# Performance work log

Measured on AMD Instinct MI355X. Metric: run time of the kernel, lower is better.

The kernel has to match this reference:

```python
import jax, jax.numpy as jnp
import numpy as np

N_HEAD = 12
N_EMBD = 768
HEAD_DIM = N_EMBD // N_HEAD
B, S = 4, 2048


def setup_inputs() -> dict:
    key = jax.random.key(0)
    k1, k2, k3, k4, k5 = jax.random.split(key, 5)
    x = jax.random.normal(k1, (B, S, N_EMBD), dtype=jnp.float32)
    # causal additive mask: 1.0 where attention is disallowed (strictly upper triangle)
    mask = (1.0 - jnp.tril(jnp.ones((S, S), dtype=jnp.float32)))[None, None, :, :]
    scale = 0.02
    W_attn = jax.random.normal(k2, (N_EMBD, 3 * N_EMBD), dtype=jnp.float32) * scale
    b_attn = jnp.zeros((3 * N_EMBD,), dtype=jnp.float32)
    W_proj = jax.random.normal(k3, (N_EMBD, N_EMBD), dtype=jnp.float32) * scale
    b_proj = jnp.zeros((N_EMBD,), dtype=jnp.float32)
    return {"x": x, "mask": mask, "W_attn": W_attn, "b_attn": b_attn,
            "W_proj": W_proj, "b_proj": b_proj}


def reference(x, mask, W_attn, b_attn, W_proj, b_proj):
    Bn, Sn, _ = x.shape
    qkv = x @ W_attn + b_attn                      # [B,S,3E]
    q, k, v = jnp.split(qkv, 3, axis=-1)           # each [B,S,E]

    def heads(t):
        return t.reshape(Bn, Sn, N_HEAD, HEAD_DIM).transpose(0, 2, 1, 3)  # [B,H,S,D]

    q, k, v = heads(q), heads(k), heads(v)
    attn = jnp.einsum('bhqd,bhkd->bhqk', q, k) / jnp.sqrt(jnp.float32(HEAD_DIM))
    attn = attn + mask * (-1e9)
    attn = jax.nn.softmax(attn, axis=-1)
    # dropout in inference mode = identity
    out = jnp.einsum('bhqk,bhkd->bhqd', attn, v)   # [B,H,S,D]
    out = out.transpose(0, 2, 1, 3).reshape(Bn, Sn, N_EMBD)
    return out @ W_proj + b_proj
```

## Files before the change

kernel.cpp:

```cpp
#include <hip/hip_runtime.h>
#include <stdint.h>

#define NHEAD 12
#define HDIM  64
#define EMB   768
#define N3    2304
#define SEQ   2048
#define BATCH 4
#define MROWS 8192

#define QSCALE 0.18033688011112042f

typedef __bf16 bf16_t;
typedef __bf16 bf16x8 __attribute__((ext_vector_type(8)));
typedef __bf16 bf16x4 __attribute__((ext_vector_type(4)));
typedef short  s16x4  __attribute__((ext_vector_type(4)));
typedef float  f32x4  __attribute__((ext_vector_type(4)));

__device__ __forceinline__ void gld_lds16(void* lds, const void* g) {
    __builtin_amdgcn_global_load_lds((const __attribute__((address_space(1))) void*)g,
                                     (__attribute__((address_space(3))) void*)lds,
                                     16, 0, 0);
}

__device__ __forceinline__ float fast_exp2(float x) {
    return __builtin_amdgcn_exp2f(x);
}

__device__ __forceinline__ f32x4 mfma16_bf16(bf16x4 a, bf16x4 b, f32x4 c) {
#if __has_builtin(__builtin_amdgcn_mfma_f32_16x16x16_bf16)
    return __builtin_amdgcn_mfma_f32_16x16x16_bf16(a, b, c, 0, 0, 0);
#else
    union U { bf16x4 h; s16x4 s; };
    U ua, ub; ua.h = a; ub.h = b;
    return __builtin_amdgcn_mfma_f32_16x16x16bf16_1k(ua.s, ub.s, c, 0, 0, 0);
#endif
}

__global__ __launch_bounds__(256) void cvt_x_k(const float* __restrict__ x,
                                               bf16_t* __restrict__ xb, int n8) {
    int idx    = blockIdx.x * blockDim.x + threadIdx.x;
    int stride = gridDim.x * blockDim.x;
    for (int i = idx; i < n8; i += stride) {
        float4 a = ((const float4*)x)[i * 2];
        float4 b = ((const float4*)x)[i * 2 + 1];
        bf16x8 v;
        v[0] = (bf16_t)a.x; v[1] = (bf16_t)a.y; v[2] = (bf16_t)a.z; v[3] = (bf16_t)a.w;
        v[4] = (bf16_t)b.x; v[5] = (bf16_t)b.y; v[6] = (bf16_t)b.z; v[7] = (bf16_t)b.w;
        ((bf16x8*)xb)[i] = v;
    }
}

__global__ __launch_bounds__(256) void transpose_cvt_k(
    const float* __restrict__ W, bf16_t* __restrict__ WT, int K, int N) {
    __shared__ float tile[32][33];
    const int n0 = blockIdx.x * 32, k0 = blockIdx.y * 32;
    const int tx = threadIdx.x & 31, ty = threadIdx.x >> 5;
#pragma unroll
    for (int i = 0; i < 32; i += 8)
        tile[ty + i][tx] = W[(size_t)(k0 + ty + i) * N + (n0 + tx)];
    __syncthreads();
#pragma unroll
    for (int i = 0; i < 32; i += 8)
        WT[(size_t)(n0 + ty + i) * K + (k0 + tx)] = (bf16_t)tile[tx][ty + i];
}

template<int MODE>
__global__ __launch_bounds__(256) void gemm_kernel(
    const bf16_t* __restrict__ Av,
    const bf16_t* __restrict__ BT,
    const float* __restrict__ bias,
    float* __restrict__ out,
    bf16_t* __restrict__ qbuf,
    bf16_t* __restrict__ kbuf,
    bf16_t* __restrict__ vbuf,
    int Ncols)
{
    const int K = 768;
    __shared__ alignas(16) bf16_t As[2][128 * 32];
    __shared__ alignas(16) bf16_t Bs[2][128 * 32];

    const int tid    = threadIdx.x;
    const int wave   = tid >> 6;
    const int lane   = tid & 63;
    const int lane15 = lane & 15;
    const int quad   = lane >> 4;

    const int bid   = blockIdx.x;
    const int chunk = (int)(gridDim.x >> 3);
    const int swz   = (bid & 7) * chunk + (bid >> 3);
    const int NB    = Ncols >> 7;
    const int mBase = (swz / NB) * 128;
    const int nBase = (swz % NB) * 128;

    const int wm = (wave >> 1) * 64;
    const int wn = (wave & 1) * 64;

    f32x4 acc[4][4];
#pragma unroll
    for (int i = 0; i < 4; i++)
#pragma unroll
        for (int j = 0; j < 4; j++) acc[i][j] = (f32x4){0.f, 0.f, 0.f, 0.f};

    const bf16_t* aSrc = Av + (size_t)mBase * K;
    const bf16_t* bSrc = BT + (size_t)nBase * K;

    const int srow = lane >> 2;
    const int sch  = lane & 3;

    auto issueA = [&](int k0, int buf) {
#pragma unroll
        for (int p = 0; p < 2; p++) {
            int r0  = p * 64 + wave * 16;
            int row = r0 + srow;
            int lch = sch ^ (row & 3);
            gld_lds16(&As[buf][r0 * 32], aSrc + (size_t)row * K + k0 + lch * 8);
        }
    };
    auto issueB = [&](int k0, int buf) {
#pragma unroll
        for (int p = 0; p < 2; p++) {
            int r0  = p * 64 + wave * 16;
            int row = r0 + srow;
            int lch = sch ^ (row & 3);
            gld_lds16(&Bs[buf][r0 * 32], bSrc + (size_t)row * K + k0 + lch * 8);
        }
    };

    issueA(0, 0);
    issueB(0, 0);

    for (int k0 = 0, it = 0; k0 < K; k0 += 32, it++) {
        const int buf = it & 1;
        __syncthreads();
        if (k0 + 32 < K) {
            issueB(k0 + 32, buf ^ 1);
            issueA(k0 + 32, buf ^ 1);
        }

        bf16x8 aF[4], bF[4];
#pragma unroll
        for (int t = 0; t < 4; t++) {
            int ra = wm + t * 16 + lane15;
            int rb = wn + t * 16 + lane15;
            aF[t] = *(const bf16x8*)&As[buf][ra * 32 + (quad ^ (ra & 3)) * 8];
            bF[t] = *(const bf16x8*)&Bs[buf][rb * 32 + (quad ^ (rb & 3)) * 8];
        }
#pragma unroll
        for (int i = 0; i < 4; i++)
#pragma unroll
            for (int j = 0; j < 4; j++)
                acc[i][j] = __builtin_amdgcn_mfma_f32_16x16x32_bf16(aF[i], bF[j], acc[i][j], 0, 0, 0);
    }

    const int region = (MODE == 1) ? (nBase / EMB) : 0;
#pragma unroll
    for (int i = 0; i < 4; i++) {
#pragma unroll
        for (int j = 0; j < 4; j++) {
            int gn = nBase + wn + j * 16 + lane15;
            float bv = bias[gn];
            if (MODE == 0) {
#pragma unroll
                for (int r = 0; r < 4; r++) {
                    int gm = mBase + wm + i * 16 + quad * 4 + r;
                    out[(size_t)gm * Ncols + gn] = acc[i][j][r] + bv;
                }
            } else if (region == 2) {
                int within = gn - 2 * EMB;
                int h = within >> 6, d = within & 63;
                int gm0 = mBase + wm + i * 16 + quad * 4;
                int b = gm0 >> 11, s = gm0 & 2047;
                int bh = b * NHEAD + h;
                bf16x4 v4;
#pragma unroll
                for (int r = 0; r < 4; r++) v4[r] = (bf16_t)(acc[i][j][r] + bv);
                *(bf16x4*)&vbuf[((size_t)bh * HDIM + d) * SEQ + s] = v4;
            } else {
                bf16_t* dst = (region == 0) ? qbuf : kbuf;
                const float scale = (region == 0) ? QSCALE : 1.0f;
                int within = gn - region * EMB;
                int h = within >> 6, d = within & 63;
#pragma unroll
                for (int r = 0; r < 4; r++) {
                    int gm = mBase + wm + i * 16 + quad * 4 + r;
                    int b = gm >> 11, s = gm & 2047;
                    int bh = b * NHEAD + h;
                    dst[((size_t)bh * SEQ + s) * HDIM + d] = (bf16_t)((acc[i][j][r] + bv) * scale);
                }
            }
        }
    }
}

__global__ __launch_bounds__(256) void attn_kernel(
    const bf16_t* __restrict__ qbuf,
    const bf16_t* __restrict__ kbuf,
    const bf16_t* __restrict__ vtbuf,
    bf16_t* __restrict__ obuf)
{
    __shared__ alignas(16) bf16_t Ks[2][64 * 64];
    __shared__ alignas(16) bf16_t Vs[2][64 * 64];
    __shared__ alignas(16) bf16_t Plds[4][16 * 72];

    const int tid    = threadIdx.x;
    const int wave   = tid >> 6;
    const int lane   = tid & 63;
    const int lane15 = lane & 15;
    const int quad   = lane >> 4;

    const int bid = blockIdx.x;
    const int swz = (bid & 7) * 96 + (bid >> 3);
    const int bh = swz >> 4;
    const int j  = swz & 15;

    const bf16_t* Qp = qbuf  + (size_t)bh * SEQ * HDIM;
    const bf16_t* Kp = kbuf  + (size_t)bh * SEQ * HDIM;
    const bf16_t* Vp = vtbuf + (size_t)bh * HDIM * SEQ;
    bf16_t* pl = &Plds[wave][0];
    const int b = bh / NHEAD, h = bh % NHEAD;

    const int srow8 = lane >> 3;
    const int sch8  = lane & 7;

    auto issueKV = [&](int kb, int buf) {
#pragma unroll
        for (int p = 0; p < 2; p++) {
            int r0  = p * 32 + wave * 8;
            int row = r0 + srow8;
            int lch = sch8 ^ (row & 7);
            gld_lds16(&Ks[buf][r0 * 64], Kp + (size_t)(kb + row) * HDIM + lch * 8);
            gld_lds16(&Vs[buf][r0 * 64], Vp + (size_t)row * SEQ + kb + lch * 8);
        }
    };

    for (int seg = 0; seg < 2; seg++) {
        const int qt = seg ? (31 - j) : j;
        const int q0 = qt * 64 + wave * 16;

        const bf16x8 qf0 = *(const bf16x8*)&Qp[(size_t)(q0 + lane15) * HDIM + quad * 8];
        const bf16x8 qf1 = *(const bf16x8*)&Qp[(size_t)(q0 + lane15) * HDIM + 32 + quad * 8];

        float lrow = 0.f;
        f32x4 oT[4];
#pragma unroll
        for (int t = 0; t < 4; t++) oT[t] = (f32x4){0.f, 0.f, 0.f, 0.f};

        const int nT = qt + 1;
        __syncthreads();
        issueKV(0, 0);

        for (int kt = 0; kt < nT; kt++) {
            const int buf = kt & 1;
            __syncthreads();
            if (kt + 1 < nT) issueKV((kt + 1) * 64, buf ^ 1);

            const int kb = kt * 64;

            f32x4 sT[4];
#pragma unroll
            for (int kg = 0; kg < 4; kg++) {
                sT[kg] = (f32x4){0.f, 0.f, 0.f, 0.f};
                int row = kg * 16 + lane15;
                bf16x8 kf0 = *(const bf16x8*)&Ks[buf][row * 64 + ((quad    ) ^ (row & 7)) * 8];
                bf16x8 kf1 = *(const bf16x8*)&Ks[buf][row * 64 + ((quad + 4) ^ (row & 7)) * 8];
                sT[kg] = __builtin_amdgcn_mfma_f32_16x16x32_bf16(kf0, qf0, sT[kg], 0, 0, 0);
                sT[kg] = __builtin_amdgcn_mfma_f32_16x16x32_bf16(kf1, qf1, sT[kg], 0, 0, 0);
            }

            if (kb + 64 > q0) {
                const int query = q0 + lane15;
#pragma unroll
                for (int kg = 0; kg < 4; kg++) {
                    int key0 = kb + kg * 16 + quad * 4;
#pragma unroll
                    for (int r = 0; r < 4; r++)
                        sT[kg][r] = (key0 + r <= query) ? sT[kg][r] : -1e30f;
                }
            }

            bf16x4 pf[4];
#pragma unroll
            for (int kg = 0; kg < 4; kg++) {
#pragma unroll
                for (int r = 0; r < 4; r++) sT[kg][r] = fast_exp2(sT[kg][r]);
                lrow += (sT[kg][0] + sT[kg][1]) + (sT[kg][2] + sT[kg][3]);
                bf16x4 v;
#pragma unroll
                for (int r = 0; r < 4; r++) v[r] = (bf16_t)sT[kg][r];
                pf[kg] = v;
            }

#pragma unroll
            for (int t = 0; t < 4; t++) {
                int vrow = t * 16 + lane15;
#pragma unroll
                for (int kg = 0; kg < 4; kg++) {
                    int c    = kg * 2 + (quad >> 1);
                    int phys = c ^ (vrow & 7);
                    bf16x4 vf = *(const bf16x4*)&Vs[buf][vrow * 64 + phys * 8 + (quad & 1) * 4];
                    oT[t] = mfma16_bf16(vf, pf[kg], oT[t]);
                }
            }
        }

        lrow += __shfl_xor(lrow, 16, 64);
        lrow += __shfl_xor(lrow, 32, 64);
        const float inv = 1.0f / lrow;

#pragma unroll
        for (int t = 0; t < 4; t++)
#pragma unroll
            for (int r = 0; r < 4; r++)
                pl[lane15 * 72 + t * 16 + quad * 4 + r] = (bf16_t)(oT[t][r] * inv);

        const int qrow = lane >> 2;
        const int ch   = lane & 3;
        bf16_t* orow = &obuf[((size_t)(b * SEQ + q0 + qrow)) * EMB + h * HDIM];
#pragma unroll
        for (int p = 0; p < 2; p++) {
            bf16x8 v = *(const bf16x8*)&pl[qrow * 72 + (ch + p * 4) * 8];
            *(bf16x8*)&orow[(ch + p * 4) * 8] = v;
        }
    }
}

extern "C" void kernel_launch(void* const* d_in, const int* in_sizes, int n_in,
                              void* d_out, int out_size, void* d_ws, size_t ws_size,
                              hipStream_t stream) {
    const float* x      = (const float*)d_in[0];
    const float* W_attn = (const float*)d_in[2];
    const float* b_attn = (const float*)d_in[3];
    const float* W_proj = (const float*)d_in[4];
    const float* b_proj = (const float*)d_in[5];
    float* out = (float*)d_out;

    bf16_t* ws  = (bf16_t*)d_ws;
    bf16_t* WaT = ws;
    bf16_t* WpT = WaT + (size_t)N3 * EMB;
    bf16_t* Qb  = WpT + (size_t)EMB * EMB;
    bf16_t* Kb  = Qb + (size_t)BATCH * NHEAD * SEQ * HDIM;
    bf16_t* Vt  = Kb + (size_t)BATCH * NHEAD * SEQ * HDIM;
    bf16_t* Ob  = Vt + (size_t)BATCH * NHEAD * SEQ * HDIM;
    bf16_t* xb  = Ob;

    transpose_cvt_k<<<dim3(N3 / 32, EMB / 32), 256, 0, stream>>>(W_attn, WaT, EMB, N3);
    transpose_cvt_k<<<dim3(EMB / 32, EMB / 32), 256, 0, stream>>>(W_proj, WpT, EMB, EMB);
    cvt_x_k<<<1536, 256, 0, stream>>>(x, xb, MROWS * EMB / 8);

    gemm_kernel<1><<<1152, 256, 0, stream>>>(
        xb, WaT, b_attn, nullptr, Qb, Kb, Vt, N3);

    attn_kernel<<<BATCH * NHEAD * 16, 256, 0, stream>>>(Qb, Kb, Vt, Ob);

    gemm_kernel<0><<<384, 256, 0, stream>>>(
        Ob, WpT, b_proj, out, nullptr, nullptr, nullptr, EMB);
}
```

Measured before the change: 223.3 us.

## Add dedicated 64x128-tile output projection kernel and MFMA priority hints in attention

Replaces the generic output-projection GEMM (128x128 tiles, 384 blocks) with a dedicated kernel using 64x128 tiles over 768 blocks, with a swizzled block order, so more workgroups fill the CUs on the small N=768 GEMM. The QKV GEMM loses its MODE 0 path. Separately, the attention kernel wraps its two MFMA sections in s_setprio(1)/s_setprio(0) so waves issuing matrix ops get scheduling priority over waves doing softmax. Smaller tiles reduce per-block data reuse and raise total global loads for the projection.

New measurement: 223.9 us. About the same (+0.3%).

```diff
diff --git a/kernel.cpp b/kernel.cpp
--- a/kernel.cpp
+++ b/kernel.cpp
@@ -153,20 +153,14 @@
                 acc[i][j] = __builtin_amdgcn_mfma_f32_16x16x32_bf16(aF[i], bF[j], acc[i][j], 0, 0, 0);
     }
 
-    const int region = (MODE == 1) ? (nBase / EMB) : 0;
+    const int region = nBase / EMB;
 #pragma unroll
     for (int i = 0; i < 4; i++) {
 #pragma unroll
         for (int j = 0; j < 4; j++) {
             int gn = nBase + wn + j * 16 + lane15;
             float bv = bias[gn];
-            if (MODE == 0) {
-#pragma unroll
-                for (int r = 0; r < 4; r++) {
-                    int gm = mBase + wm + i * 16 + quad * 4 + r;
-                    out[(size_t)gm * Ncols + gn] = acc[i][j][r] + bv;
-                }
-            } else if (region == 2) {
+            if (region == 2) {
                 int within = gn - 2 * EMB;
                 int h = within >> 6, d = within & 63;
                 int gm0 = mBase + wm + i * 16 + quad * 4;
@@ -188,6 +182,99 @@
                     int bh = b * NHEAD + h;
                     dst[((size_t)bh * SEQ + s) * HDIM + d] = (bf16_t)((acc[i][j][r] + bv) * scale);
                 }
+            }
+        }
+    }
+}
+
+__global__ __launch_bounds__(256) void proj_kernel(
+    const bf16_t* __restrict__ Av,
+    const bf16_t* __restrict__ BT,
+    const float*  __restrict__ bias,
+    float* __restrict__ out)
+{
+    const int K = 768;
+    __shared__ alignas(16) bf16_t As[2][64 * 32];
+    __shared__ alignas(16) bf16_t Bs[2][128 * 32];
+
+    const int tid    = threadIdx.x;
+    const int wave   = tid >> 6;
+    const int lane   = tid & 63;
+    const int lane15 = lane & 15;
+    const int quad   = lane >> 4;
+
+    const int bid   = blockIdx.x;
+    const int swz   = (bid & 7) * 96 + (bid >> 3);
+    const int mBase = (swz / 6) * 64;
+    const int nBase = (swz % 6) * 128;
+
+    f32x4 acc[4][2];
+#pragma unroll
+    for (int t = 0; t < 4; t++)
+#pragma unroll
+        for (int u = 0; u < 2; u++) acc[t][u] = (f32x4){0.f, 0.f, 0.f, 0.f};
+
+    const bf16_t* aSrc = Av + (size_t)mBase * K;
+    const bf16_t* bSrc = BT + (size_t)nBase * K;
+
+    const int srow = lane >> 2;
+    const int sch  = lane & 3;
+
+    auto issueA = [&](int k0, int buf) {
+        int r0  = wave * 16;
+        int row = r0 + srow;
+        int lch = sch ^ (row & 3);
+        gld_lds16(&As[buf][r0 * 32], aSrc + (size_t)row * K + k0 + lch * 8);
+    };
+    auto issueB = [&](int k0, int buf) {
+#pragma unroll
+        for (int p = 0; p < 2; p++) {
+            int r0  = p * 64 + wave * 16;
+            int row = r0 + srow;
+            int lch = sch ^ (row & 3);
+            gld_lds16(&Bs[buf][r0 * 32], bSrc + (size_t)row * K + k0 + lch * 8);
+        }
+    };
+
+    issueA(0, 0);
+    issueB(0, 0);
+
+    for (int k0 = 0, it = 0; k0 < K; k0 += 32, it++) {
+        const int buf = it & 1;
+        __syncthreads();
+        if (k0 + 32 < K) {
+            issueB(k0 + 32, buf ^ 1);
+            issueA(k0 + 32, buf ^ 1);
+        }
+
+        bf16x8 aF[4], bF[2];
+#pragma unroll
+        for (int t = 0; t < 4; t++) {
+            int ra = t * 16 + lane15;
+            aF[t] = *(const bf16x8*)&As[buf][ra * 32 + (quad ^ (ra & 3)) * 8];
+        }
+#pragma unroll
+        for (int u = 0; u < 2; u++) {
+            int rb = wave * 32 + u * 16 + lane15;
+            bF[u] = *(const bf16x8*)&Bs[buf][rb * 32 + (quad ^ (rb & 3)) * 8];
+        }
+#pragma unroll
+        for (int t = 0; t < 4; t++)
+#pragma unroll
+            for (int u = 0; u < 2; u++)
+                acc[t][u] = __builtin_amdgcn_mfma_f32_16x16x32_bf16(aF[t], bF[u], acc[t][u], 0, 0, 0);
+    }
+
+#pragma unroll
+    for (int t = 0; t < 4; t++) {
+#pragma unroll
+        for (int u = 0; u < 2; u++) {
+            int gn = nBase + wave * 32 + u * 16 + lane15;
+            float bv = bias[gn];
+#pragma unroll
+            for (int r = 0; r < 4; r++) {
+                int gm = mBase + t * 16 + quad * 4 + r;
+                out[(size_t)gm * EMB + gn] = acc[t][u][r] + bv;
             }
         }
     }
@@ -258,6 +345,7 @@
             const int kb = kt * 64;
 
             f32x4 sT[4];
+            __builtin_amdgcn_s_setprio(1);
 #pragma unroll
             for (int kg = 0; kg < 4; kg++) {
                 sT[kg] = (f32x4){0.f, 0.f, 0.f, 0.f};
@@ -267,6 +355,7 @@
                 sT[kg] = __builtin_amdgcn_mfma_f32_16x16x32_bf16(kf0, qf0, sT[kg], 0, 0, 0);
                 sT[kg] = __builtin_amdgcn_mfma_f32_16x16x32_bf16(kf1, qf1, sT[kg], 0, 0, 0);
             }
+            __builtin_amdgcn_s_setprio(0);
 
             if (kb + 64 > q0) {
                 const int query = q0 + lane15;
@@ -291,6 +380,7 @@
                 pf[kg] = v;
             }
 
+            __builtin_amdgcn_s_setprio(1);
 #pragma unroll
             for (int t = 0; t < 4; t++) {
                 int vrow = t * 16 + lane15;
@@ -302,6 +392,7 @@
                     oT[t] = mfma16_bf16(vf, pf[kg], oT[t]);
                 }
             }
+            __builtin_amdgcn_s_setprio(0);
         }
 
         lrow += __shfl_xor(lrow, 16, 64);
@@ -353,6 +444,5 @@
 
     attn_kernel<<<BATCH * NHEAD * 16, 256, 0, stream>>>(Qb, Kb, Vt, Ob);
 
-    gemm_kernel<0><<<384, 256, 0, stream>>>(
-        Ob, WpT, b_proj, out, nullptr, nullptr, nullptr, EMB);
-}
+    proj_kernel<<<768, 256, 0, stream>>>(Ob, WpT, b_proj, out);
+}
```
